# Kernel optimization log

Measured on AMD Instinct MI355X. Metric: run time of the kernel, lower is better.

## Reference

```python
import jax, jax.numpy as jnp
import numpy as np

DIM = 1024
NUM_HEADS = 16
HEAD_DIM = DIM // NUM_HEADS
SCALE = HEAD_DIM ** -0.5


def setup_inputs() -> dict:
    key = jax.random.key(0)
    k1, k2, k3 = jax.random.split(key, 3)
    B, N = 2, 2048
    x = jax.random.normal(k1, (B, N, DIM), dtype=jnp.float32)
    w_qkv = jax.random.normal(k2, (3 * DIM, DIM), dtype=jnp.float32) * (DIM ** -0.5)
    w_proj = jax.random.normal(k3, (DIM, DIM), dtype=jnp.float32) * (DIM ** -0.5)
    b_proj = jnp.zeros((DIM,), dtype=jnp.float32)
    return {"x": x, "w_qkv": w_qkv, "w_proj": w_proj, "b_proj": b_proj}


def reference(x, w_qkv, w_proj, b_proj):
    B, N, C = x.shape
    # qkv projection (no bias): [B,N,3C] -> [3,B,H,N,Dh]
    qkv = jnp.einsum('bnc,dc->bnd', x, w_qkv)
    qkv = qkv.reshape(B, N, 3, NUM_HEADS, HEAD_DIM).transpose(2, 0, 3, 1, 4)
    q, k, v = qkv[0], qkv[1], qkv[2]
    # scaled dot-product attention (full score matrix, as in source)
    attn = jnp.einsum('bhnd,bhmd->bhnm', q * SCALE, k)
    attn = jax.nn.softmax(attn, axis=-1)
    out = jnp.einsum('bhnm,bhmd->bhnd', attn, v)  # [B,H,N,Dh]
    out = out.transpose(0, 2, 1, 3).reshape(B, N, C)
    return out @ w_proj.T + b_proj
```

## Files before the change

kernel.cpp:

```cpp
#include <hip/hip_runtime.h>

#define DIM   1024
#define NH    16
#define HD    64
#define BATCH 2
#define SEQ   2048
#define MTOT  4096
#define SCALE 0.125f
#define LOG2E 1.44269504088896340736f

typedef __attribute__((ext_vector_type(8))) short short8_t;
typedef __attribute__((ext_vector_type(4))) short short4_t;
typedef __attribute__((ext_vector_type(4))) float f32x4;

__device__ __forceinline__ float4 ld4(const float* p) { return *(const float4*)p; }

__device__ __forceinline__ unsigned short f2bf(float f) {
    unsigned u = __float_as_uint(f);
    unsigned r = u + 0x7FFF + ((u >> 16) & 1);
    return (unsigned short)(r >> 16);
}

__device__ __forceinline__ void gl2lds16(const void* g, void* l) {
    __builtin_amdgcn_global_load_lds(
        (const __attribute__((address_space(1))) unsigned int*)g,
        (__attribute__((address_space(3))) unsigned int*)l, 16, 0, 0);
}

__global__ __launch_bounds__(256) void cvt3(const float* __restrict__ x,
                                            const float* __restrict__ wq,
                                            const float* __restrict__ wp,
                                            unsigned short* __restrict__ xb,
                                            unsigned short* __restrict__ wqb,
                                            unsigned short* __restrict__ wpb) {
    size_t i = ((size_t)blockIdx.x * 256 + threadIdx.x) * 4;
    if (i < (size_t)MTOT * DIM) {
        float4 t = ld4(x + i);
        ushort4 o = {f2bf(t.x), f2bf(t.y), f2bf(t.z), f2bf(t.w)};
        *(ushort4*)(xb + i) = o;
    }
    if (i < (size_t)3 * DIM * DIM) {
        float4 t = ld4(wq + i);
        ushort4 o = {f2bf(t.x), f2bf(t.y), f2bf(t.z), f2bf(t.w)};
        *(ushort4*)(wqb + i) = o;
    }
    if (i < (size_t)DIM * DIM) {
        float4 t = ld4(wp + i);
        ushort4 o = {f2bf(t.x), f2bf(t.y), f2bf(t.z), f2bf(t.w)};
        *(ushort4*)(wpb + i) = o;
    }
}

__device__ __forceinline__ void gemm128_core(const unsigned short* __restrict__ A,
                                             const unsigned short* __restrict__ B,
                                             int m0, int n0, int K,
                                             unsigned short* As, unsigned short* Bs,
                                             f32x4 acc[4][4]) {
    const int tid  = threadIdx.x;
    const int w    = tid >> 6;
    const int lane = tid & 63;
    const int g = lane >> 4, c = lane & 15;
    const int wr = w >> 1, wc = w & 1;

    const int srow = lane >> 2;
    const int j    = (lane & 3) ^ ((lane >> 4) & 3);
    const unsigned short* ga0 = A + (size_t)(m0 + w * 32 + srow) * K + j * 8;
    const unsigned short* ga1 = ga0 + (size_t)16 * K;
    const unsigned short* gb0 = B + (size_t)(n0 + w * 32 + srow) * K + j * 8;
    const unsigned short* gb1 = gb0 + (size_t)16 * K;
    unsigned short* la0 = As + w * 1024;
    unsigned short* la1 = la0 + 512;
    unsigned short* lb0 = Bs + w * 1024;
    unsigned short* lb1 = lb0 + 512;

    const int swz = (g ^ ((c >> 2) & 3)) * 8;
    int aoff[4], boff[4];
    #pragma unroll
    for (int t = 0; t < 4; ++t) {
        aoff[t] = (wr * 64 + t * 16 + c) * 32 + swz;
        boff[t] = (wc * 64 + t * 16 + c) * 32 + swz;
    }

    for (int kb = 0; kb < K; kb += 32) {
        if (kb) __syncthreads();
        gl2lds16(ga0 + kb, la0);
        gl2lds16(ga1 + kb, la1);
        gl2lds16(gb0 + kb, lb0);
        gl2lds16(gb1 + kb, lb1);
        __syncthreads();
        short8_t af[4], bf[4];
        #pragma unroll
        for (int t = 0; t < 4; ++t) af[t] = *(const short8_t*)&As[aoff[t]];
        #pragma unroll
        for (int t = 0; t < 4; ++t) bf[t] = *(const short8_t*)&Bs[boff[t]];
        #pragma unroll
        for (int rt = 0; rt < 4; ++rt)
            #pragma unroll
            for (int ct = 0; ct < 4; ++ct)
                acc[rt][ct] = __builtin_amdgcn_mfma_f32_16x16x32_bf16(
                    af[rt], bf[ct], acc[rt][ct], 0, 0, 0);
    }
}

__global__ __launch_bounds__(256) void qkv_mfma(const unsigned short* __restrict__ xb,
                                                const unsigned short* __restrict__ wqb,
                                                unsigned short* __restrict__ q,
                                                unsigned short* __restrict__ k,
                                                unsigned short* __restrict__ v) {
    __shared__ unsigned short As[128 * 32];
    __shared__ unsigned short Bs[128 * 32];
    const int m0 = blockIdx.x * 128;
    const int n0 = blockIdx.y * 128;
    f32x4 acc[4][4];
    #pragma unroll
    for (int i = 0; i < 4; ++i)
        #pragma unroll
        for (int jj = 0; jj < 4; ++jj) acc[i][jj] = (f32x4){0.f, 0.f, 0.f, 0.f};

    gemm128_core(xb, wqb, m0, n0, DIM, As, Bs, acc);

    const int tid = threadIdx.x, w = tid >> 6, lane = tid & 63;
    const int g = lane >> 4, c = lane & 15;
    const int wr = w >> 1, wc = w & 1;
    const int which = n0 >> 10;
    const int hh    = ((n0 + wc * 64) & 1023) >> 6;
    const int b     = m0 >> 11;
    unsigned short* dst  = (which == 0) ? q : (which == 1) ? k : v;
    unsigned short* base = dst + (size_t)(b * NH + hh) * SEQ * HD;
    const float sc = (which == 0) ? SCALE * LOG2E : 1.0f;
    #pragma unroll
    for (int rt = 0; rt < 4; ++rt)
        #pragma unroll
        for (int ct = 0; ct < 4; ++ct)
            #pragma unroll
            for (int r = 0; r < 4; ++r) {
                int row = (m0 + wr * 64 + rt * 16 + g * 4 + r) & 2047;
                base[(size_t)row * HD + ct * 16 + c] = f2bf(acc[rt][ct][r] * sc);
            }
}

__global__ __launch_bounds__(256) void proj_mfma(const unsigned short* __restrict__ aob,
                                                 const unsigned short* __restrict__ wpb,
                                                 const float* __restrict__ bias,
                                                 float* __restrict__ out) {
    __shared__ unsigned short As[128 * 32];
    __shared__ unsigned short Bs[128 * 32];
    const int m0 = blockIdx.x * 128;
    const int n0 = blockIdx.y * 128;
    f32x4 acc[4][4];
    #pragma unroll
    for (int i = 0; i < 4; ++i)
        #pragma unroll
        for (int jj = 0; jj < 4; ++jj) acc[i][jj] = (f32x4){0.f, 0.f, 0.f, 0.f};

    gemm128_core(aob, wpb, m0, n0, DIM, As, Bs, acc);

    const int tid = threadIdx.x, w = tid >> 6, lane = tid & 63;
    const int g = lane >> 4, c = lane & 15;
    const int wr = w >> 1, wc = w & 1;
    float br[4];
    #pragma unroll
    for (int ct = 0; ct < 4; ++ct) br[ct] = bias[n0 + wc * 64 + ct * 16 + c];
    #pragma unroll
    for (int rt = 0; rt < 4; ++rt)
        #pragma unroll
        for (int ct = 0; ct < 4; ++ct)
            #pragma unroll
            for (int r = 0; r < 4; ++r) {
                int row = m0 + wr * 64 + rt * 16 + g * 4 + r;
                out[(size_t)row * DIM + n0 + wc * 64 + ct * 16 + c] =
                    acc[rt][ct][r] + br[ct];
            }
}

__global__ __launch_bounds__(256) void vtrans(const unsigned short* __restrict__ v,
                                              unsigned short* __restrict__ vt) {
    __shared__ unsigned short Ts[64 * 72];
    const int tid = threadIdx.x;
    const int bh = blockIdx.y;
    const int n0 = blockIdx.x * 64;
    const int r    = tid >> 2;
    const int cseg = (tid & 3) * 16;
    const unsigned short* src = v + ((size_t)bh * SEQ + n0 + r) * HD + cseg;
    uint4 a  = *(const uint4*)src;
    uint4 b2 = *(const uint4*)(src + 8);
    *(uint4*)&Ts[r * 72 + cseg]     = a;
    *(uint4*)&Ts[r * 72 + cseg + 8] = b2;
    __syncthreads();
    const int d    = tid >> 2;
    const int nseg = (tid & 3) * 16;
    unsigned short tmp[16];
    #pragma unroll
    for (int jj = 0; jj < 16; ++jj) tmp[jj] = Ts[(nseg + jj) * 72 + d];
    unsigned short* dstp = vt + ((size_t)bh * HD + d) * SEQ + n0 + nseg;
    *(uint4*)dstp       = *(uint4*)&tmp[0];
    *(uint4*)(dstp + 8) = *(uint4*)&tmp[8];
}

__global__ __launch_bounds__(256) void attn_mfma(const unsigned short* __restrict__ q,
                                                 const unsigned short* __restrict__ k,
                                                 const unsigned short* __restrict__ vt,
                                                 unsigned short* __restrict__ aob) {
    __shared__ unsigned short Ks[64 * 64];
    __shared__ unsigned short Vs[64 * 64];

    const int tid  = threadIdx.x;
    const int w    = tid >> 6;
    const int lane = tid & 63;
    const int g    = lane >> 4;
    const int c    = lane & 15;
    const int qt = blockIdx.x, bh = blockIdx.y;
    const int b = bh >> 4, h = bh & 15;
    const int q0 = qt * 128 + w * 32;

    const unsigned short* qbase = q + ((size_t)bh * SEQ + q0) * HD;
    short8_t qf[2][2];
    #pragma unroll
    for (int s = 0; s < 2; ++s) {
        const unsigned short* qr = qbase + (size_t)(s * 16 + c) * HD + g * 8;
        qf[s][0] = *(const short8_t*)qr;
        qf[s][1] = *(const short8_t*)(qr + 32);
    }

    f32x4 o[2][4];
    #pragma unroll
    for (int s = 0; s < 2; ++s)
        #pragma unroll
        for (int dt = 0; dt < 4; ++dt) o[s][dt] = (f32x4){0.f, 0.f, 0.f, 0.f};
    float rs0 = 0.f, rs1 = 0.f;

    const int r8 = lane >> 3;
    const int js = lane & 7;
    const int j0 = js ^ r8;
    const unsigned short* kg = k  + (size_t)bh * SEQ * HD + (size_t)(w * 16 + r8) * HD + j0 * 8;
    const unsigned short* vg = vt + (size_t)bh * HD * SEQ + (size_t)(w * 16 + r8) * SEQ + j0 * 8;
    unsigned short* lK = Ks + w * 16 * 64;
    unsigned short* lV = Vs + w * 16 * 64;

    int koff[4];
    #pragma unroll
    for (int ct = 0; ct < 4; ++ct)
        koff[ct] = (ct * 16 + c) * 64 + ((g ^ (c & 7)) * 8);

    for (int kt = 0; kt < 32; ++kt) {
        if (kt) __syncthreads();
        gl2lds16(kg + (size_t)kt * 4096,                lK);
        gl2lds16(kg + (size_t)kt * 4096 + 8 * HD,       lK + 512);
        gl2lds16(vg + (size_t)kt * 64,                  lV);
        gl2lds16(vg + (size_t)kt * 64 + 8 * SEQ,        lV + 512);
        __syncthreads();

        f32x4 s0[4], s1[4];
        #pragma unroll
        for (int ct = 0; ct < 4; ++ct) {
            short8_t kf0 = *(const short8_t*)&Ks[koff[ct]];
            short8_t kf1 = *(const short8_t*)&Ks[koff[ct] ^ 32];
            s0[ct] = __builtin_amdgcn_mfma_f32_16x16x32_bf16(kf0, qf[0][0],
                         (f32x4){0.f, 0.f, 0.f, 0.f}, 0, 0, 0);
            s0[ct] = __builtin_amdgcn_mfma_f32_16x16x32_bf16(kf1, qf[0][1], s0[ct], 0, 0, 0);
            s1[ct] = __builtin_amdgcn_mfma_f32_16x16x32_bf16(kf0, qf[1][0],
                         (f32x4){0.f, 0.f, 0.f, 0.f}, 0, 0, 0);
            s1[ct] = __builtin_amdgcn_mfma_f32_16x16x32_bf16(kf1, qf[1][1], s1[ct], 0, 0, 0);
        }

        short4_t pf0[4], pf1[4];
        #pragma unroll
        for (int ct = 0; ct < 4; ++ct) {
            #pragma unroll
            for (int r = 0; r < 4; ++r) {
                float p0 = exp2f(s0[ct][r]); rs0 += p0; pf0[ct][r] = (short)f2bf(p0);
                float p1 = exp2f(s1[ct][r]); rs1 += p1; pf1[ct][r] = (short)f2bf(p1);
            }
        }

        #pragma unroll
        for (int dt = 0; dt < 4; ++dt) {
            #pragma unroll
            for (int kt2 = 0; kt2 < 4; ++kt2) {
                int voff = (dt * 16 + c) * 64 +
                           (((2 * kt2 + (g >> 1)) ^ (c & 7)) * 8) + 4 * (g & 1);
                short4_t vf = *(const short4_t*)&Vs[voff];
                o[0][dt] = __builtin_amdgcn_mfma_f32_16x16x16bf16_1k(vf, pf0[kt2], o[0][dt], 0, 0, 0);
                o[1][dt] = __builtin_amdgcn_mfma_f32_16x16x16bf16_1k(vf, pf1[kt2], o[1][dt], 0, 0, 0);
            }
        }
    }

    rs0 += __shfl_xor(rs0, 16); rs0 += __shfl_xor(rs0, 32);
    rs1 += __shfl_xor(rs1, 16); rs1 += __shfl_xor(rs1, 32);
    const float inv[2] = {1.0f / rs0, 1.0f / rs1};

    #pragma unroll
    for (int s = 0; s < 2; ++s) {
        unsigned short* orow = aob + ((size_t)b * SEQ + q0 + s * 16 + c) * DIM + h * HD;
        #pragma unroll
        for (int dt = 0; dt < 4; ++dt) {
            ushort4 ov;
            ov.x = f2bf(o[s][dt][0] * inv[s]);
            ov.y = f2bf(o[s][dt][1] * inv[s]);
            ov.z = f2bf(o[s][dt][2] * inv[s]);
            ov.w = f2bf(o[s][dt][3] * inv[s]);
            *(ushort4*)&orow[dt * 16 + 4 * g] = ov;
        }
    }
}

extern "C" void kernel_launch(void* const* d_in, const int* in_sizes, int n_in,
                              void* d_out, int out_size, void* d_ws, size_t ws_size,
                              hipStream_t stream) {
    const float* x      = (const float*)d_in[0];
    const float* w_qkv  = (const float*)d_in[1];
    const float* w_proj = (const float*)d_in[2];
    const float* b_proj = (const float*)d_in[3];
    float* out = (float*)d_out;

    const size_t per = (size_t)BATCH * NH * SEQ * HD;
    const size_t nwq = (size_t)3 * DIM * DIM;
    const size_t nwp = (size_t)DIM * DIM;
    const size_t need = (6 * per + nwq + nwp) * sizeof(unsigned short);
    if (ws_size < need) return;

    unsigned short* q   = (unsigned short*)d_ws;
    unsigned short* k   = q + per;
    unsigned short* v   = k + per;
    unsigned short* vt  = v + per;
    unsigned short* aob = vt + per;
    unsigned short* xb  = aob + per;
    unsigned short* wqb = xb + per;
    unsigned short* wpb = wqb + nwq;

    cvt3<<<dim3(4096), 256, 0, stream>>>(x, w_qkv, w_proj, xb, wqb, wpb);
    qkv_mfma<<<dim3(32, 24), 256, 0, stream>>>(xb, wqb, q, k, v);
    vtrans<<<dim3(32, 32), 256, 0, stream>>>(v, vt);
    attn_mfma<<<dim3(16, 32), 256, 0, stream>>>(q, k, vt, aob);
    proj_mfma<<<dim3(32, 8), 256, 0, stream>>>(aob, wpb, b_proj, out);
}
```

Before: 212.8 us.

## Switch to fp16 MFMA, fuse V transpose into QKV epilogue, use fast exp2

The bf16 pipeline becomes fp16 throughout, which lets the code use hardware packed conversion (cvt_pkrtz) instead of manual bf16 rounding in the softmax and epilogues. The V transpose kernel is removed: the QKV GEMM epilogue writes V directly in transposed layout with 4-element vector stores, saving a launch and a round trip through memory. The softmax uses the native exp2 builtin. The risks are fp16 range and precision limits, and strided transposed stores in the QKV epilogue.

New measurement: 188.0 us. 1.13x faster.

```diff
diff --git a/kernel.cpp b/kernel.cpp
--- a/kernel.cpp
+++ b/kernel.cpp
@@ -9,16 +9,26 @@
 #define SCALE 0.125f
 #define LOG2E 1.44269504088896340736f
 
-typedef __attribute__((ext_vector_type(8))) short short8_t;
-typedef __attribute__((ext_vector_type(4))) short short4_t;
+typedef __attribute__((ext_vector_type(8))) _Float16 half8_t;
+typedef __attribute__((ext_vector_type(4))) _Float16 half4_t;
+typedef __attribute__((ext_vector_type(2))) __fp16 pk16x2_t;
 typedef __attribute__((ext_vector_type(4))) float f32x4;
 
+union H4 { pk16x2_t h2[2]; half4_t h4; ushort4 us; };
+
 __device__ __forceinline__ float4 ld4(const float* p) { return *(const float4*)p; }
 
-__device__ __forceinline__ unsigned short f2bf(float f) {
-    unsigned u = __float_as_uint(f);
-    unsigned r = u + 0x7FFF + ((u >> 16) & 1);
-    return (unsigned short)(r >> 16);
+__device__ __forceinline__ unsigned short f2h(float f) {
+    _Float16 h = (_Float16)f;
+    return *(unsigned short*)&h;
+}
+
+__device__ __forceinline__ float fast_exp2(float x) {
+#if __has_builtin(__builtin_amdgcn_exp2f)
+    return __builtin_amdgcn_exp2f(x);
+#else
+    return exp2f(x);
+#endif
 }
 
 __device__ __forceinline__ void gl2lds16(const void* g, void* l) {
@@ -30,24 +40,24 @@
 __global__ __launch_bounds__(256) void cvt3(const float* __restrict__ x,
                                             const float* __restrict__ wq,
                                             const float* __restrict__ wp,
-                                            unsigned short* __restrict__ xb,
-                                            unsigned short* __restrict__ wqb,
-                                            unsigned short* __restrict__ wpb) {
+                                            unsigned short* __restrict__ xh,
+                                            unsigned short* __restrict__ wqh,
+                                            unsigned short* __restrict__ wph) {
     size_t i = ((size_t)blockIdx.x * 256 + threadIdx.x) * 4;
     if (i < (size_t)MTOT * DIM) {
         float4 t = ld4(x + i);
-        ushort4 o = {f2bf(t.x), f2bf(t.y), f2bf(t.z), f2bf(t.w)};
-        *(ushort4*)(xb + i) = o;
+        ushort4 o = {f2h(t.x), f2h(t.y), f2h(t.z), f2h(t.w)};
+        *(ushort4*)(xh + i) = o;
     }
     if (i < (size_t)3 * DIM * DIM) {
         float4 t = ld4(wq + i);
-        ushort4 o = {f2bf(t.x), f2bf(t.y), f2bf(t.z), f2bf(t.w)};
-        *(ushort4*)(wqb + i) = o;
+        ushort4 o = {f2h(t.x), f2h(t.y), f2h(t.z), f2h(t.w)};
+        *(ushort4*)(wqh + i) = o;
     }
     if (i < (size_t)DIM * DIM) {
         float4 t = ld4(wp + i);
-        ushort4 o = {f2bf(t.x), f2bf(t.y), f2bf(t.z), f2bf(t.w)};
-        *(ushort4*)(wpb + i) = o;
+        ushort4 o = {f2h(t.x), f2h(t.y), f2h(t.z), f2h(t.w)};
+        *(ushort4*)(wph + i) = o;
     }
 }
 
@@ -88,25 +98,25 @@
         gl2lds16(gb0 + kb, lb0);
         gl2lds16(gb1 + kb, lb1);
         __syncthreads();
-        short8_t af[4], bf[4];
-        #pragma unroll
-        for (int t = 0; t < 4; ++t) af[t] = *(const short8_t*)&As[aoff[t]];
-        #pragma unroll
-        for (int t = 0; t < 4; ++t) bf[t] = *(const short8_t*)&Bs[boff[t]];
+        half8_t af[4], bf[4];
+        #pragma unroll
+        for (int t = 0; t < 4; ++t) af[t] = *(const half8_t*)&As[aoff[t]];
+        #pragma unroll
+        for (int t = 0; t < 4; ++t) bf[t] = *(const half8_t*)&Bs[boff[t]];
         #pragma unroll
         for (int rt = 0; rt < 4; ++rt)
             #pragma unroll
             for (int ct = 0; ct < 4; ++ct)
-                acc[rt][ct] = __builtin_amdgcn_mfma_f32_16x16x32_bf16(
+                acc[rt][ct] = __builtin_amdgcn_mfma_f32_16x16x32_f16(
                     af[rt], bf[ct], acc[rt][ct], 0, 0, 0);
     }
 }
 
-__global__ __launch_bounds__(256) void qkv_mfma(const unsigned short* __restrict__ xb,
-                                                const unsigned short* __restrict__ wqb,
+__global__ __launch_bounds__(256) void qkv_mfma(const unsigned short* __restrict__ xh,
+                                                const unsigned short* __restrict__ wqh,
                                                 unsigned short* __restrict__ q,
                                                 unsigned short* __restrict__ k,
-                                                unsigned short* __restrict__ v) {
+                                                unsigned short* __restrict__ vt) {
     __shared__ unsigned short As[128 * 32];
     __shared__ unsigned short Bs[128 * 32];
     const int m0 = blockIdx.x * 128;
@@ -117,7 +127,7 @@
         #pragma unroll
         for (int jj = 0; jj < 4; ++jj) acc[i][jj] = (f32x4){0.f, 0.f, 0.f, 0.f};
 
-    gemm128_core(xb, wqb, m0, n0, DIM, As, Bs, acc);
+    gemm128_core(xh, wqh, m0, n0, DIM, As, Bs, acc);
 
     const int tid = threadIdx.x, w = tid >> 6, lane = tid & 63;
     const int g = lane >> 4, c = lane & 15;
@@ -125,22 +135,38 @@
     const int which = n0 >> 10;
     const int hh    = ((n0 + wc * 64) & 1023) >> 6;
     const int b     = m0 >> 11;
-    unsigned short* dst  = (which == 0) ? q : (which == 1) ? k : v;
-    unsigned short* base = dst + (size_t)(b * NH + hh) * SEQ * HD;
-    const float sc = (which == 0) ? SCALE * LOG2E : 1.0f;
-    #pragma unroll
-    for (int rt = 0; rt < 4; ++rt)
-        #pragma unroll
-        for (int ct = 0; ct < 4; ++ct)
-            #pragma unroll
-            for (int r = 0; r < 4; ++r) {
-                int row = (m0 + wr * 64 + rt * 16 + g * 4 + r) & 2047;
-                base[(size_t)row * HD + ct * 16 + c] = f2bf(acc[rt][ct][r] * sc);
+    const int nb    = m0 & 2047;
+
+    if (which == 2) {
+        unsigned short* base = vt + (size_t)(b * NH + hh) * HD * SEQ;
+        #pragma unroll
+        for (int rt = 0; rt < 4; ++rt)
+            #pragma unroll
+            for (int ct = 0; ct < 4; ++ct) {
+                int n4 = nb + wr * 64 + rt * 16 + 4 * g;
+                H4 u;
+                u.h2[0] = __builtin_amdgcn_cvt_pkrtz(acc[rt][ct][0], acc[rt][ct][1]);
+                u.h2[1] = __builtin_amdgcn_cvt_pkrtz(acc[rt][ct][2], acc[rt][ct][3]);
+                *(ushort4*)&base[(size_t)(ct * 16 + c) * SEQ + n4] = u.us;
             }
-}
-
-__global__ __launch_bounds__(256) void proj_mfma(const unsigned short* __restrict__ aob,
-                                                 const unsigned short* __restrict__ wpb,
+    } else {
+        unsigned short* dst  = (which == 0) ? q : k;
+        unsigned short* base = dst + (size_t)(b * NH + hh) * SEQ * HD;
+        const float sc = (which == 0) ? SCALE * LOG2E : 1.0f;
+        #pragma unroll
+        for (int rt = 0; rt < 4; ++rt)
+            #pragma unroll
+            for (int ct = 0; ct < 4; ++ct)
+                #pragma unroll
+                for (int r = 0; r < 4; ++r) {
+                    int row = nb + wr * 64 + rt * 16 + g * 4 + r;
+                    base[(size_t)row * HD + ct * 16 + c] = f2h(acc[rt][ct][r] * sc);
+                }
+    }
+}
+
+__global__ __launch_bounds__(256) void proj_mfma(const unsigned short* __restrict__ aoh,
+                                                 const unsigned short* __restrict__ wph,
                                                  const float* __restrict__ bias,
                                                  float* __restrict__ out) {
     __shared__ unsigned short As[128 * 32];
@@ -153,7 +179,7 @@
         #pragma unroll
         for (int jj = 0; jj < 4; ++jj) acc[i][jj] = (f32x4){0.f, 0.f, 0.f, 0.f};
 
-    gemm128_core(aob, wpb, m0, n0, DIM, As, Bs, acc);
+    gemm128_core(aoh, wph, m0, n0, DIM, As, Bs, acc);
 
     const int tid = threadIdx.x, w = tid >> 6, lane = tid & 63;
     const int g = lane >> 4, c = lane & 15;
@@ -173,34 +199,10 @@
             }
 }
 
-__global__ __launch_bounds__(256) void vtrans(const unsigned short* __restrict__ v,
-                                              unsigned short* __restrict__ vt) {
-    __shared__ unsigned short Ts[64 * 72];
-    const int tid = threadIdx.x;
-    const int bh = blockIdx.y;
-    const int n0 = blockIdx.x * 64;
-    const int r    = tid >> 2;
-    const int cseg = (tid & 3) * 16;
-    const unsigned short* src = v + ((size_t)bh * SEQ + n0 + r) * HD + cseg;
-    uint4 a  = *(const uint4*)src;
-    uint4 b2 = *(const uint4*)(src + 8);
-    *(uint4*)&Ts[r * 72 + cseg]     = a;
-    *(uint4*)&Ts[r * 72 + cseg + 8] = b2;
-    __syncthreads();
-    const int d    = tid >> 2;
-    const int nseg = (tid & 3) * 16;
-    unsigned short tmp[16];
-    #pragma unroll
-    for (int jj = 0; jj < 16; ++jj) tmp[jj] = Ts[(nseg + jj) * 72 + d];
-    unsigned short* dstp = vt + ((size_t)bh * HD + d) * SEQ + n0 + nseg;
-    *(uint4*)dstp       = *(uint4*)&tmp[0];
-    *(uint4*)(dstp + 8) = *(uint4*)&tmp[8];
-}
-
 __global__ __launch_bounds__(256) void attn_mfma(const unsigned short* __restrict__ q,
                                                  const unsigned short* __restrict__ k,
                                                  const unsigned short* __restrict__ vt,
-                                                 unsigned short* __restrict__ aob) {
+                                                 unsigned short* __restrict__ aoh) {
     __shared__ unsigned short Ks[64 * 64];
     __shared__ unsigned short Vs[64 * 64];
 
@@ -214,12 +216,12 @@
     const int q0 = qt * 128 + w * 32;
 
     const unsigned short* qbase = q + ((size_t)bh * SEQ + q0) * HD;
-    short8_t qf[2][2];
+    half8_t qf[2][2];
     #pragma unroll
     for (int s = 0; s < 2; ++s) {
         const unsigned short* qr = qbase + (size_t)(s * 16 + c) * HD + g * 8;
-        qf[s][0] = *(const short8_t*)qr;
-        qf[s][1] = *(const short8_t*)(qr + 32);
+        qf[s][0] = *(const half8_t*)qr;
+        qf[s][1] = *(const half8_t*)(qr + 32);
     }
 
     f32x4 o[2][4];
@@ -244,33 +246,40 @@
 
     for (int kt = 0; kt < 32; ++kt) {
         if (kt) __syncthreads();
-        gl2lds16(kg + (size_t)kt * 4096,                lK);
-        gl2lds16(kg + (size_t)kt * 4096 + 8 * HD,       lK + 512);
-        gl2lds16(vg + (size_t)kt * 64,                  lV);
-        gl2lds16(vg + (size_t)kt * 64 + 8 * SEQ,        lV + 512);
+        gl2lds16(kg + (size_t)kt * 4096,          lK);
+        gl2lds16(kg + (size_t)kt * 4096 + 8 * HD, lK + 512);
+        gl2lds16(vg + (size_t)kt * 64,            lV);
+        gl2lds16(vg + (size_t)kt * 64 + 8 * SEQ,  lV + 512);
         __syncthreads();
 
         f32x4 s0[4], s1[4];
         #pragma unroll
         for (int ct = 0; ct < 4; ++ct) {
-            short8_t kf0 = *(const short8_t*)&Ks[koff[ct]];
-            short8_t kf1 = *(const short8_t*)&Ks[koff[ct] ^ 32];
-            s0[ct] = __builtin_amdgcn_mfma_f32_16x16x32_bf16(kf0, qf[0][0],
+            half8_t kf0 = *(const half8_t*)&Ks[koff[ct]];
+            half8_t kf1 = *(const half8_t*)&Ks[koff[ct] ^ 32];
+            s0[ct] = __builtin_amdgcn_mfma_f32_16x16x32_f16(kf0, qf[0][0],
                          (f32x4){0.f, 0.f, 0.f, 0.f}, 0, 0, 0);
-            s0[ct] = __builtin_amdgcn_mfma_f32_16x16x32_bf16(kf1, qf[0][1], s0[ct], 0, 0, 0);
-            s1[ct] = __builtin_amdgcn_mfma_f32_16x16x32_bf16(kf0, qf[1][0],
+            s0[ct] = __builtin_amdgcn_mfma_f32_16x16x32_f16(kf1, qf[0][1], s0[ct], 0, 0, 0);
+            s1[ct] = __builtin_amdgcn_mfma_f32_16x16x32_f16(kf0, qf[1][0],
                          (f32x4){0.f, 0.f, 0.f, 0.f}, 0, 0, 0);
-            s1[ct] = __builtin_amdgcn_mfma_f32_16x16x32_bf16(kf1, qf[1][1], s1[ct], 0, 0, 0);
+            s1[ct] = __builtin_amdgcn_mfma_f32_16x16x32_f16(kf1, qf[1][1], s1[ct], 0, 0, 0);
         }
 
-        short4_t pf0[4], pf1[4];
+        half4_t pf0[4], pf1[4];
         #pragma unroll
         for (int ct = 0; ct < 4; ++ct) {
-            #pragma unroll
-            for (int r = 0; r < 4; ++r) {
-                float p0 = exp2f(s0[ct][r]); rs0 += p0; pf0[ct][r] = (short)f2bf(p0);
-                float p1 = exp2f(s1[ct][r]); rs1 += p1; pf1[ct][r] = (short)f2bf(p1);
-            }
+            float a0 = fast_exp2(s0[ct][0]), a1 = fast_exp2(s0[ct][1]);
+            float a2 = fast_exp2(s0[ct][2]), a3 = fast_exp2(s0[ct][3]);
+            rs0 += (a0 + a1) + (a2 + a3);
+            H4 u0; u0.h2[0] = __builtin_amdgcn_cvt_pkrtz(a0, a1);
+                   u0.h2[1] = __builtin_amdgcn_cvt_pkrtz(a2, a3);
+            pf0[ct] = u0.h4;
+            float b0 = fast_exp2(s1[ct][0]), b1 = fast_exp2(s1[ct][1]);
+            float b2 = fast_exp2(s1[ct][2]), b3 = fast_exp2(s1[ct][3]);
+            rs1 += (b0 + b1) + (b2 + b3);
+            H4 u1; u1.h2[0] = __builtin_amdgcn_cvt_pkrtz(b0, b1);
+                   u1.h2[1] = __builtin_amdgcn_cvt_pkrtz(b2, b3);
+            pf1[ct] = u1.h4;
         }
 
         #pragma unroll
@@ -279,9 +288,9 @@
             for (int kt2 = 0; kt2 < 4; ++kt2) {
                 int voff = (dt * 16 + c) * 64 +
                            (((2 * kt2 + (g >> 1)) ^ (c & 7)) * 8) + 4 * (g & 1);
-                short4_t vf = *(const short4_t*)&Vs[voff];
-                o[0][dt] = __builtin_amdgcn_mfma_f32_16x16x16bf16_1k(vf, pf0[kt2], o[0][dt], 0, 0, 0);
-                o[1][dt] = __builtin_amdgcn_mfma_f32_16x16x16bf16_1k(vf, pf1[kt2], o[1][dt], 0, 0, 0);
+                half4_t vf = *(const half4_t*)&Vs[voff];
+                o[0][dt] = __builtin_amdgcn_mfma_f32_16x16x16f16(vf, pf0[kt2], o[0][dt], 0, 0, 0);
+                o[1][dt] = __builtin_amdgcn_mfma_f32_16x16x16f16(vf, pf1[kt2], o[1][dt], 0, 0, 0);
             }
         }
     }
@@ -292,15 +301,13 @@
 
     #pragma unroll
     for (int s = 0; s < 2; ++s) {
-        unsigned short* orow = aob + ((size_t)b * SEQ + q0 + s * 16 + c) * DIM + h * HD;
+        unsigned short* orow = aoh + ((size_t)b * SEQ + q0 + s * 16 + c) * DIM + h * HD;
         #pragma unroll
         for (int dt = 0; dt < 4; ++dt) {
-            ushort4 ov;
-            ov.x = f2bf(o[s][dt][0] * inv[s]);
-            ov.y = f2bf(o[s][dt][1] * inv[s]);
-            ov.z = f2bf(o[s][dt][2] * inv[s]);
-            ov.w = f2bf(o[s][dt][3] * inv[s]);
-            *(ushort4*)&orow[dt * 16 + 4 * g] = ov;
+            H4 u;
+            u.h2[0] = __builtin_amdgcn_cvt_pkrtz(o[s][dt][0] * inv[s], o[s][dt][1] * inv[s]);
+            u.h2[1] = __builtin_amdgcn_cvt_pkrtz(o[s][dt][2] * inv[s], o[s][dt][3] * inv[s]);
+            *(ushort4*)&orow[dt * 16 + 4 * g] = u.us;
         }
     }
 }
@@ -317,21 +324,19 @@
     const size_t per = (size_t)BATCH * NH * SEQ * HD;
     const size_t nwq = (size_t)3 * DIM * DIM;
     const size_t nwp = (size_t)DIM * DIM;
-    const size_t need = (6 * per + nwq + nwp) * sizeof(unsigned short);
+    const size_t need = (5 * per + nwq + nwp) * sizeof(unsigned short);
     if (ws_size < need) return;
 
     unsigned short* q   = (unsigned short*)d_ws;
     unsigned short* k   = q + per;
-    unsigned short* v   = k + per;
-    unsigned short* vt  = v + per;
-    unsigned short* aob = vt + per;
-    unsigned short* xb  = aob + per;
-    unsigned short* wqb = xb + per;
-    unsigned short* wpb = wqb + nwq;
-
-    cvt3<<<dim3(4096), 256, 0, stream>>>(x, w_qkv, w_proj, xb, wqb, wpb);
-    qkv_mfma<<<dim3(32, 24), 256, 0, stream>>>(xb, wqb, q, k, v);
-    vtrans<<<dim3(32, 32), 256, 0, stream>>>(v, vt);
-    attn_mfma<<<dim3(16, 32), 256, 0, stream>>>(q, k, vt, aob);
-    proj_mfma<<<dim3(32, 8), 256, 0, stream>>>(aob, wpb, b_proj, out);
-}
+    unsigned short* vt  = k + per;
+    unsigned short* aoh = vt + per;
+    unsigned short* xh  = aoh + per;
+    unsigned short* wqh = xh + per;
+    unsigned short* wph = wqh + nwq;
+
+    cvt3<<<dim3(4096), 256, 0, stream>>>(x, w_qkv, w_proj, xh, wqh, wph);
+    qkv_mfma<<<dim3(32, 24), 256, 0, stream>>>(xh, wqh, q, k, vt);
+    attn_mfma<<<dim3(16, 32), 256, 0, stream>>>(q, k, vt, aoh);
+    proj_mfma<<<dim3(32, 8), 256, 0, stream>>>(aoh, wph, b_proj, out);
+}
```
